# Performance work log

Measured on AMD Instinct MI355X. Metric: run time of the kernel, lower is better.

The kernel has to match this reference:

```python
import jax, jax.numpy as jnp
import numpy as np
from jax import lax

B, T, D = 2, 512, 64   # batch, temporal length, input_dim
H = 64                 # hidden_dims
OUT = 64               # output_dim
REL = 2 * D            # relation_dim = input_dim * 2 (until=True: max & min interval pooling)


def _interval_pool(f, op):
    """f: [B,T,D] -> r: [B,T,T,D] with r[:, i, j] = op-reduction of f[:, i..j] for i <= j.
    Entries with i > j are filled with f[:, i] (degenerate interval); they are never
    read because the downstream backward pooling only reduces over j >= i."""
    Tn = f.shape[1]
    idx = jnp.arange(Tn)

    def step(col, j):
        # col[:, i] holds reduce(f[:, i..j-1]) for i <= j-1, and f[:, i] otherwise
        new = op(col, f[:, j][:, None, :])                      # extend interval to j
        new = jnp.where((idx <= j)[None, :, None], new, f)      # reset i > j rows
        return new, new

    _, cols = lax.scan(step, f, jnp.arange(Tn))  # [T(j), B, T(i), D]
    return jnp.transpose(cols, (1, 2, 0, 3))     # [B, T(i), T(j), D]


def _backward_max_pool(s):
    """s: [B,T,T,C] -> out[:, i] = max_{j >= i} s[:, i, j]  (the 'broadcast' backward pool)."""
    Tn = s.shape[1]
    mask = jnp.arange(Tn)[:, None] <= jnp.arange(Tn)[None, :]   # i <= j
    neg = jnp.asarray(-1e9, s.dtype)
    return jnp.max(jnp.where(mask[None, :, :, None], s, neg), axis=2)


def setup_inputs() -> dict:
    key = jax.random.key(0)
    ks = jax.random.split(key, 7)
    f = jax.random.normal(ks[0], (B, T, D), dtype=jnp.float32)
    # step_linears per __init__: current_dim starts at REL, then hidden_dims
    dims = [(REL + REL, H), (H + REL, H), (H + REL, OUT)]
    params = {}
    for i, (din, dout) in enumerate(dims):
        params[f"W{i}"] = jax.random.normal(ks[1 + 2 * i], (din, dout), jnp.float32) / np.sqrt(din)
        params[f"b{i}"] = jnp.zeros((dout,), jnp.float32)
    return {"f": f, **params}


def reference(f, W0, b0, W1, b1, W2, b2):
    Tn = f.shape[1]
    # until=True: concat max- and min-interval pooling -> [B,T,T,2D]
    r = jnp.concatenate([_interval_pool(f, jnp.maximum),
                         _interval_pool(f, jnp.minimum)], axis=-1)
    current = r[:, :, Tn - 1]  # [B, T, REL] : reductions over suffix intervals [i, T-1]
    for W, b in ((W0, b0), (W1, b1), (W2, b2)):
        # jactorch.add_dim(current, 1, t): broadcast current (indexed by j) over new i axis
        bcast = jnp.broadcast_to(current[:, None, :, :],
                                 (f.shape[0], Tn, Tn, current.shape[-1]))
        li = jnp.concatenate([bcast, r], axis=-1)                 # [B,T,T,C+REL]
        h = jax.nn.sigmoid(jnp.einsum('bijc,co->bijo', li, W) + b)  # MLPLogic, no hidden layers
        current = _backward_max_pool(h)                           # [B,T,out]
    return current
```

## Files before the change

kernel.cpp:

```cpp
#include <hip/hip_runtime.h>
#include <hip/hip_bf16.h>
#include <math.h>

#define B_ 2
#define T_ 512
#define D_ 64
#define NBLK_PER_B 1088

typedef __attribute__((ext_vector_type(8))) short bf16x8;
typedef __attribute__((ext_vector_type(8))) unsigned short u16x8;
typedef __attribute__((ext_vector_type(4))) float f32x4;

static __device__ __forceinline__ unsigned short f2bf(float v) {
    __hip_bfloat16 h = __float2bfloat16(v);
    return *reinterpret_cast<unsigned short*>(&h);
}
static __device__ __forceinline__ float bf2f(unsigned short u) {
    return __uint_as_float(((unsigned)u) << 16);
}
static __device__ __forceinline__ unsigned short maxbits(unsigned short a, unsigned short b) {
    float m = fmaxf(bf2f(a), bf2f(b));
    return (unsigned short)(__float_as_uint(m) >> 16);
}
static __device__ __forceinline__ unsigned short minbits(unsigned short a, unsigned short b) {
    float m = fminf(bf2f(a), bf2f(b));
    return (unsigned short)(__float_as_uint(m) >> 16);
}

__global__ __launch_bounds__(512) void prep_kernel(
    const float* __restrict__ f,
    const float* __restrict__ W0, const float* __restrict__ W1, const float* __restrict__ W2,
    unsigned short* __restrict__ tmax, unsigned short* __restrict__ tmin,
    unsigned short* __restrict__ wf,
    unsigned short* __restrict__ cur0bf, unsigned short* __restrict__ intra,
    float* __restrict__ z0, float* __restrict__ z1, float* __restrict__ z2) {

    __shared__ unsigned short lmax[512][16];
    __shared__ unsigned short lmin[512][16];

    const int blk = blockIdx.x;
    const int tid = threadIdx.x;

    if (blk < 8) {
        const int b = blk & 1;
        const int c0 = (blk >> 1) * 16;
        const int t = tid;

        u16x8 mx[2], mn[2];
#pragma unroll
        for (int h = 0; h < 2; ++h) {
            const float* fp = &f[((size_t)(b * T_ + t) << 6) + c0 + h * 8];
#pragma unroll
            for (int e = 0; e < 8; ++e) {
                unsigned short u = f2bf(fp[e]);
                mx[h][e] = u; mn[h][e] = u;
            }
            size_t base = ((size_t)(b * T_ + t) << 6) + c0 + h * 8;
            *reinterpret_cast<u16x8*>(&tmax[base]) = mx[h];
            *reinterpret_cast<u16x8*>(&tmin[base]) = mn[h];
        }
        for (int k = 1; k <= 9; ++k) {
            *reinterpret_cast<u16x8*>(&lmax[t][0]) = mx[0];
            *reinterpret_cast<u16x8*>(&lmax[t][8]) = mx[1];
            *reinterpret_cast<u16x8*>(&lmin[t][0]) = mn[0];
            *reinterpret_cast<u16x8*>(&lmin[t][8]) = mn[1];
            __syncthreads();
            int t2 = t + (1 << (k - 1));
            if (t2 > T_ - 1) t2 = T_ - 1;
            u16x8 qx0 = *reinterpret_cast<const u16x8*>(&lmax[t2][0]);
            u16x8 qx1 = *reinterpret_cast<const u16x8*>(&lmax[t2][8]);
            u16x8 qn0 = *reinterpret_cast<const u16x8*>(&lmin[t2][0]);
            u16x8 qn1 = *reinterpret_cast<const u16x8*>(&lmin[t2][8]);
#pragma unroll
            for (int e = 0; e < 8; ++e) {
                mx[0][e] = maxbits(mx[0][e], qx0[e]);
                mx[1][e] = maxbits(mx[1][e], qx1[e]);
                mn[0][e] = minbits(mn[0][e], qn0[e]);
                mn[1][e] = minbits(mn[1][e], qn1[e]);
            }
            size_t base = ((size_t)((k * B_ + b) * T_ + t) << 6) + c0;
            *reinterpret_cast<u16x8*>(&tmax[base]) = mx[0];
            *reinterpret_cast<u16x8*>(&tmax[base + 8]) = mx[1];
            *reinterpret_cast<u16x8*>(&tmin[base]) = mn[0];
            *reinterpret_cast<u16x8*>(&tmin[base + 8]) = mn[1];
            __syncthreads();
        }
    } else if (blk < 11) {
        const int layer = blk - 8;
        const float* W = (layer == 0) ? W0 : ((layer == 1) ? W1 : W2);
        const int FRS = (layer == 0) ? 32 : 24;
        const int l = tid & 63;
        for (int fr = tid >> 6; fr < FRS; fr += 8) {
            int kt = fr >> 2, nt = fr & 3;
#pragma unroll
            for (int e = 0; e < 8; ++e) {
                int row = kt * 32 + ((l >> 4) << 3) + e;
                int col = nt * 16 + (l & 15);
                wf[((size_t)(layer * 32 + fr) * 64 + l) * 8 + e] = f2bf(W[row * 64 + col]);
            }
        }
    } else if (blk < 139) {
        const int x = blk - 11;
        const int c = x & 63, b = x >> 6;
        const int t = tid;
        float* smax = reinterpret_cast<float*>(lmax);
        float* smin = reinterpret_cast<float*>(lmin);
        float v = f[((size_t)(b * T_ + t) << 6) + c];
        smax[t] = v; smin[t] = v;
        __syncthreads();
        for (int off = 1; off < 512; off <<= 1) {
            float a = (t + off < 512) ? smax[t + off] : -1e30f;
            float m = (t + off < 512) ? smin[t + off] : 1e30f;
            __syncthreads();
            smax[t] = fmaxf(smax[t], a);
            smin[t] = fminf(smin[t], m);
            __syncthreads();
        }
        cur0bf[((size_t)(b * T_ + t) << 7) + c] = f2bf(smax[t]);
        cur0bf[((size_t)(b * T_ + t) << 7) + 64 + c] = f2bf(smin[t]);
    } else if (blk < 171) {
        const int x = blk - 139;
        const int jt = x & 15, b = x >> 4;
        const int jj = tid >> 4, c8 = tid & 15;
        const bool ismin = c8 >= 8;
        unsigned short (*sc)[128] = reinterpret_cast<unsigned short (*)[128]>(lmax);

        const float* fp = &f[((size_t)(b * T_ + jt * 32 + jj) << 6) + (c8 & 7) * 8];
        u16x8 r;
#pragma unroll
        for (int e = 0; e < 8; ++e) r[e] = f2bf(fp[e]);

#pragma unroll
        for (int off = 1; off < 32; off <<= 1) {
            *reinterpret_cast<u16x8*>(&sc[jj][c8 * 8]) = r;
            __syncthreads();
            if (jj >= off) {
                u16x8 q = *reinterpret_cast<const u16x8*>(&sc[jj - off][c8 * 8]);
#pragma unroll
                for (int e = 0; e < 8; ++e)
                    r[e] = ismin ? minbits(r[e], q[e]) : maxbits(r[e], q[e]);
            }
            __syncthreads();
        }
        *reinterpret_cast<u16x8*>(&intra[((size_t)((b * 16 + jt) * 32 + jj) << 7) + c8 * 8]) = r;
    } else {
        int fi = (blk - 171) * 512 + tid;
        float4 z = {0.f, 0.f, 0.f, 0.f};
        if (fi < 16384)       reinterpret_cast<float4*>(z0)[fi] = z;
        else if (fi < 32768)  reinterpret_cast<float4*>(z1)[fi - 16384] = z;
        else                  reinterpret_cast<float4*>(z2)[fi - 32768] = z;
    }
}

template <int C, bool FROM_TAB>
__global__ __launch_bounds__(256) void pair_kernel(
    const unsigned short* __restrict__ tabmax,
    const unsigned short* __restrict__ tabmin,
    const unsigned short* __restrict__ cur0bf,
    const unsigned short* __restrict__ intra,
    const float* __restrict__ curprev,
    const unsigned short* __restrict__ wf,
    const float* __restrict__ bias,
    float* __restrict__ out) {

    constexpr int KTC = C / 32;
    constexpr int KT = KTC + 4;
    constexpr int CP = (C == 128) ? 136 : 72;

    int m = blockIdx.x;
    int b = 0;
    if (m >= NBLK_PER_B) { b = 1; m -= NBLK_PER_B; }
    int jt = 0;
    while (m >= 4 * (jt + 1) * (jt + 2)) ++jt;
    const int it = m - 4 * jt * (jt + 1);
    const bool diag = (it >= 8 * jt);
    const int i0 = it * 4, j0 = jt * 32;

    const int tid = threadIdx.x;
    const int l = tid & 63, w = tid >> 6;
    const int lg = l >> 4, li = l & 15;

    __shared__ unsigned short curl[32][CP];
    __shared__ unsigned short intr[32][136];
    __shared__ unsigned short pref[4][136];

    if (FROM_TAB) {
#pragma unroll
        for (int q = 0; q < 2; ++q) {
            int chn = q * 256 + tid;
            int jj = chn >> 4, c8 = chn & 15;
            u16x8 v = *reinterpret_cast<const u16x8*>(
                &cur0bf[((size_t)(b * T_ + j0 + jj) << 7) + c8 * 8]);
            *reinterpret_cast<u16x8*>(&curl[jj][c8 * 8]) = v;
        }
    } else {
        int jj = tid >> 3, c8 = tid & 7;
        const float* cp = &curprev[((size_t)(b * T_ + j0 + jj) << 6) + c8 * 8];
        float4 v0 = *reinterpret_cast<const float4*>(cp);
        float4 v1 = *reinterpret_cast<const float4*>(cp + 4);
        u16x8 r;
        r[0] = f2bf(v0.x); r[1] = f2bf(v0.y); r[2] = f2bf(v0.z); r[3] = f2bf(v0.w);
        r[4] = f2bf(v1.x); r[5] = f2bf(v1.y); r[6] = f2bf(v1.z); r[7] = f2bf(v1.w);
        *reinterpret_cast<u16x8*>(&curl[jj][c8 * 8]) = r;
    }

    if (!diag) {
#pragma unroll
        for (int q = 0; q < 2; ++q) {
            int chn = q * 256 + tid;
            int jj = chn >> 4, c8 = chn & 15;
            u16x8 v = *reinterpret_cast<const u16x8*>(
                &intra[((size_t)((b * 16 + jt) * 32 + jj) << 7) + c8 * 8]);
            *reinterpret_cast<u16x8*>(&intr[jj][c8 * 8]) = v;
        }
        if (tid < 64) {
            int isel = tid >> 4, c8 = tid & 15;
            int i = i0 + isel;
            int len = j0 - i;
            int kk = 31 - __clz(len);
            int t2 = j0 - (1 << kk);
            const unsigned short* tab = (c8 < 8) ? tabmax : tabmin;
            int cc = (c8 & 7) * 8;
            u16x8 va = *reinterpret_cast<const u16x8*>(&tab[(((size_t)(kk * B_ + b) * T_ + i) << 6) + cc]);
            u16x8 vb = *reinterpret_cast<const u16x8*>(&tab[(((size_t)(kk * B_ + b) * T_ + t2) << 6) + cc]);
            u16x8 r;
#pragma unroll
            for (int e = 0; e < 8; ++e)
                r[e] = (c8 < 8) ? maxbits(va[e], vb[e]) : minbits(va[e], vb[e]);
            *reinterpret_cast<u16x8*>(&pref[isel][c8 * 8]) = r;
        }
    }
    __syncthreads();

    f32x4 acc[2][4];
#pragma unroll
    for (int s = 0; s < 2; ++s)
#pragma unroll
        for (int nt = 0; nt < 4; ++nt) acc[s][nt] = (f32x4){0.f, 0.f, 0.f, 0.f};

    const int pi = i0 + w;

#pragma unroll
    for (int kt = 0; kt < KT; ++kt) {
        bf16x8 bfr[4];
#pragma unroll
        for (int nt = 0; nt < 4; ++nt)
            bfr[nt] = *reinterpret_cast<const bf16x8*>(&wf[(size_t)((kt * 4 + nt) * 64 + l) * 8]);

#pragma unroll
        for (int s = 0; s < 2; ++s) {
            const int pjj = 16 * s + li;
            bf16x8 av;
            if (kt < KTC) {
                av = *reinterpret_cast<const bf16x8*>(&curl[pjj][kt * 32 + lg * 8]);
            } else {
                const int krt = kt - KTC;
                const int c8 = krt * 4 + lg;
                if (!diag) {
                    u16x8 iv = *reinterpret_cast<const u16x8*>(&intr[pjj][c8 * 8]);
                    u16x8 pv = *reinterpret_cast<const u16x8*>(&pref[w][c8 * 8]);
#pragma unroll
                    for (int e = 0; e < 8; ++e)
                        av[e] = (short)((c8 < 8) ? maxbits(iv[e], pv[e]) : minbits(iv[e], pv[e]));
                } else {
                    const int pj = j0 + pjj;
                    const int je = (pj < pi) ? pi : pj;
                    const int len = je - pi + 1;
                    const int kk = 31 - __clz(len);
                    const int t2 = je + 1 - (1 << kk);
                    const unsigned short* tab = (c8 < 8) ? tabmax : tabmin;
                    const int cc = (c8 & 7) * 8;
                    u16x8 va = *reinterpret_cast<const u16x8*>(&tab[(((size_t)(kk * B_ + b) * T_ + pi) << 6) + cc]);
                    u16x8 vb = *reinterpret_cast<const u16x8*>(&tab[(((size_t)(kk * B_ + b) * T_ + t2) << 6) + cc]);
#pragma unroll
                    for (int e = 0; e < 8; ++e)
                        av[e] = (short)((c8 < 8) ? maxbits(va[e], vb[e]) : minbits(va[e], vb[e]));
                }
            }
#pragma unroll
            for (int nt = 0; nt < 4; ++nt)
                acc[s][nt] = __builtin_amdgcn_mfma_f32_16x16x32_bf16(av, bfr[nt], acc[s][nt], 0, 0, 0);
        }
    }

#pragma unroll
    for (int nt = 0; nt < 4; ++nt) {
        float vm = -1e9f;
#pragma unroll
        for (int s = 0; s < 2; ++s)
#pragma unroll
            for (int r = 0; r < 4; ++r) {
                int jj = 16 * s + lg * 4 + r;
                if (j0 + jj >= pi) vm = fmaxf(vm, acc[s][nt][r]);
            }
        vm = fmaxf(vm, __shfl_xor(vm, 16));
        vm = fmaxf(vm, __shfl_xor(vm, 32));
        if (l < 16) {
            int o = nt * 16 + li;
            float h = 1.0f / (1.0f + __expf(-(vm + bias[o])));
            atomicMax((int*)out + (((size_t)(b * T_ + pi) << 6) + o), __float_as_int(h));
        }
    }
}

extern "C" void kernel_launch(void* const* d_in, const int* in_sizes, int n_in,
                              void* d_out, int out_size, void* d_ws, size_t ws_size,
                              hipStream_t stream) {
    const float* f  = (const float*)d_in[0];
    const float* W0 = (const float*)d_in[1];
    const float* b0 = (const float*)d_in[2];
    const float* W1 = (const float*)d_in[3];
    const float* b1 = (const float*)d_in[4];
    const float* W2 = (const float*)d_in[5];
    const float* b2 = (const float*)d_in[6];
    float* outp = (float*)d_out;

    unsigned short* tabmax = (unsigned short*)d_ws;
    unsigned short* tabmin = tabmax + 10 * B_ * T_ * 64;
    unsigned short* wf     = tabmin + 10 * B_ * T_ * 64;
    unsigned short* cur0bf = wf + 3 * 32 * 64 * 8;
    unsigned short* intra  = cur0bf + B_ * T_ * 128;
    float* cur1 = (float*)(intra + B_ * 16 * 32 * 128);
    float* cur2 = cur1 + B_ * T_ * 64;

    prep_kernel<<<dim3(267), dim3(512), 0, stream>>>(f, W0, W1, W2,
                                                     tabmax, tabmin, wf,
                                                     cur0bf, intra,
                                                     cur1, cur2, outp);

    const dim3 pgrid(B_ * NBLK_PER_B);
    pair_kernel<128, true ><<<pgrid, dim3(256), 0, stream>>>(tabmax, tabmin, cur0bf, intra,
                                                             nullptr, wf + 0 * 32 * 64 * 8, b0, cur1);
    pair_kernel<64,  false><<<pgrid, dim3(256), 0, stream>>>(tabmax, tabmin, cur0bf, intra,
                                                             cur1, wf + 1 * 32 * 64 * 8, b1, cur2);
    pair_kernel<64,  false><<<pgrid, dim3(256), 0, stream>>>(tabmax, tabmin, cur0bf, intra,
                                                             cur2, wf + 2 * 32 * 64 * 8, b2, outp);
}
```

Before: 83.53 us.

## Stage weights in LDS, reorder block mapping, hoist diagonal index math

Each block now copies the bf16 weight fragments into shared memory once and reads MFMA B operands from LDS instead of global memory every k-step. The blockIdx mapping is reordered so that all 128 diagonal tiles per batch come first, followed by the off-diagonal tiles. Sparse-table index math for diagonal tiles is hoisted out of the k loop, max/min selection is resolved per k-tile at compile time, and the causal mask is skipped for off-diagonal tiles. The trade-off is extra LDS use and a staging load per block, which may lower occupancy.

Measured after the change: 80.57 us. 3.5% less time.

```diff
diff --git a/kernel.cpp b/kernel.cpp
--- a/kernel.cpp
+++ b/kernel.cpp
@@ -170,19 +170,37 @@
     int m = blockIdx.x;
     int b = 0;
     if (m >= NBLK_PER_B) { b = 1; m -= NBLK_PER_B; }
-    int jt = 0;
-    while (m >= 4 * (jt + 1) * (jt + 2)) ++jt;
-    const int it = m - 4 * jt * (jt + 1);
-    const bool diag = (it >= 8 * jt);
+    int jt, it;
+    bool diag;
+    if (m < 128) {
+        diag = true;
+        jt = m >> 3;
+        it = 8 * jt + (m & 7);
+    } else {
+        diag = false;
+        int m2 = m - 128;
+        jt = 1;
+        while (m2 >= 4 * jt * (jt + 1)) ++jt;
+        it = m2 - 4 * jt * (jt - 1);
+    }
     const int i0 = it * 4, j0 = jt * 32;
 
     const int tid = threadIdx.x;
     const int l = tid & 63, w = tid >> 6;
     const int lg = l >> 4, li = l & 15;
+    const int pi = i0 + w;
 
     __shared__ unsigned short curl[32][CP];
     __shared__ unsigned short intr[32][136];
     __shared__ unsigned short pref[4][136];
+    __shared__ unsigned short wlds[KT * 4 * 64 * 8];
+
+#pragma unroll
+    for (int q = 0; q < KT; ++q) {
+        int idx = q * 256 + tid;
+        u16x8 v = *reinterpret_cast<const u16x8*>(&wf[(size_t)idx * 8]);
+        *reinterpret_cast<u16x8*>(&wlds[idx * 8]) = v;
+    }
 
     if (FROM_TAB) {
 #pragma unroll
@@ -232,20 +250,30 @@
     }
     __syncthreads();
 
+    int kk_q[2], t2_q[2];
+    if (diag) {
+#pragma unroll
+        for (int s = 0; s < 2; ++s) {
+            int pj = j0 + 16 * s + li;
+            int je = (pj < pi) ? pi : pj;
+            int len = je - pi + 1;
+            kk_q[s] = 31 - __clz(len);
+            t2_q[s] = je + 1 - (1 << kk_q[s]);
+        }
+    }
+
     f32x4 acc[2][4];
 #pragma unroll
     for (int s = 0; s < 2; ++s)
 #pragma unroll
         for (int nt = 0; nt < 4; ++nt) acc[s][nt] = (f32x4){0.f, 0.f, 0.f, 0.f};
 
-    const int pi = i0 + w;
-
 #pragma unroll
     for (int kt = 0; kt < KT; ++kt) {
-        bf16x8 bfr[4];
+        bf16x8 wfr[4];
 #pragma unroll
         for (int nt = 0; nt < 4; ++nt)
-            bfr[nt] = *reinterpret_cast<const bf16x8*>(&wf[(size_t)((kt * 4 + nt) * 64 + l) * 8]);
+            wfr[nt] = *reinterpret_cast<const bf16x8*>(&wlds[((kt * 4 + nt) * 64 + l) * 8]);
 
 #pragma unroll
         for (int s = 0; s < 2; ++s) {
@@ -255,31 +283,38 @@
                 av = *reinterpret_cast<const bf16x8*>(&curl[pjj][kt * 32 + lg * 8]);
             } else {
                 const int krt = kt - KTC;
-                const int c8 = krt * 4 + lg;
                 if (!diag) {
-                    u16x8 iv = *reinterpret_cast<const u16x8*>(&intr[pjj][c8 * 8]);
-                    u16x8 pv = *reinterpret_cast<const u16x8*>(&pref[w][c8 * 8]);
-#pragma unroll
-                    for (int e = 0; e < 8; ++e)
-                        av[e] = (short)((c8 < 8) ? maxbits(iv[e], pv[e]) : minbits(iv[e], pv[e]));
+                    u16x8 iv = *reinterpret_cast<const u16x8*>(&intr[pjj][(krt * 4 + lg) * 8]);
+                    u16x8 pv = *reinterpret_cast<const u16x8*>(&pref[w][(krt * 4 + lg) * 8]);
+                    if (krt < 2) {
+#pragma unroll
+                        for (int e = 0; e < 8; ++e) av[e] = (short)maxbits(iv[e], pv[e]);
+                    } else {
+#pragma unroll
+                        for (int e = 0; e < 8; ++e) av[e] = (short)minbits(iv[e], pv[e]);
+                    }
                 } else {
-                    const int pj = j0 + pjj;
-                    const int je = (pj < pi) ? pi : pj;
-                    const int len = je - pi + 1;
-                    const int kk = 31 - __clz(len);
-                    const int t2 = je + 1 - (1 << kk);
-                    const unsigned short* tab = (c8 < 8) ? tabmax : tabmin;
+                    const int c8 = krt * 4 + lg;
+                    const unsigned short* tab = (krt < 2) ? tabmax : tabmin;
                     const int cc = (c8 & 7) * 8;
-                    u16x8 va = *reinterpret_cast<const u16x8*>(&tab[(((size_t)(kk * B_ + b) * T_ + pi) << 6) + cc]);
-                    u16x8 vb = *reinterpret_cast<const u16x8*>(&tab[(((size_t)(kk * B_ + b) * T_ + t2) << 6) + cc]);
-#pragma unroll
-                    for (int e = 0; e < 8; ++e)
-                        av[e] = (short)((c8 < 8) ? maxbits(va[e], vb[e]) : minbits(va[e], vb[e]));
+                    const int kk = kk_q[0], t2v = t2_q[0];
+                    const int kk1 = kk_q[1], t2v1 = t2_q[1];
+                    const int kku = (s == 0) ? kk : kk1;
+                    const int t2u = (s == 0) ? t2v : t2v1;
+                    u16x8 va = *reinterpret_cast<const u16x8*>(&tab[(((size_t)(kku * B_ + b) * T_ + pi) << 6) + cc]);
+                    u16x8 vb = *reinterpret_cast<const u16x8*>(&tab[(((size_t)(kku * B_ + b) * T_ + t2u) << 6) + cc]);
+                    if (krt < 2) {
+#pragma unroll
+                        for (int e = 0; e < 8; ++e) av[e] = (short)maxbits(va[e], vb[e]);
+                    } else {
+#pragma unroll
+                        for (int e = 0; e < 8; ++e) av[e] = (short)minbits(va[e], vb[e]);
+                    }
                 }
             }
 #pragma unroll
             for (int nt = 0; nt < 4; ++nt)
-                acc[s][nt] = __builtin_amdgcn_mfma_f32_16x16x32_bf16(av, bfr[nt], acc[s][nt], 0, 0, 0);
+                acc[s][nt] = __builtin_amdgcn_mfma_f32_16x16x32_bf16(av, wfr[nt], acc[s][nt], 0, 0, 0);
         }
     }
 
@@ -291,7 +326,7 @@
 #pragma unroll
             for (int r = 0; r < 4; ++r) {
                 int jj = 16 * s + lg * 4 + r;
-                if (j0 + jj >= pi) vm = fmaxf(vm, acc[s][nt][r]);
+                if (!diag || (j0 + jj >= pi)) vm = fmaxf(vm, acc[s][nt][r]);
             }
         vm = fmaxf(vm, __shfl_xor(vm, 16));
         vm = fmaxf(vm, __shfl_xor(vm, 32));
```
